# Kernel tuning notes

Measured on AMD Instinct MI355X. Metric: run time of the kernel, lower is better.

## Reference

```python
import jax, jax.numpy as jnp
import numpy as np


def _rconv(x, w, b):
    # reflection-pad 1 then 3x3 valid conv (same spatial size), NCHW/OIHW
    xp = jnp.pad(x, ((0, 0), (0, 0), (1, 1), (1, 1)), mode='reflect')
    y = jax.lax.conv_general_dilated(
        xp, w, window_strides=(1, 1), padding='VALID',
        dimension_numbers=('NCHW', 'OIHW', 'NCHW'))
    return y + b[None, :, None, None]


def setup_inputs() -> dict:
    key = jax.random.key(0)
    ks = jax.random.split(key, 12)
    B, C, H, W = 4, 256, 64, 64
    IC = 128  # inter_channels
    s = lambda fan_in: 1.0 / np.sqrt(fan_in)
    return {
        'query_feat': jax.random.normal(ks[0], (B, C, H, W), jnp.float32),
        'key_feat': jax.random.normal(ks[1], (B, C, H, W), jnp.float32),
        # 1x1 conv projections (stored as [out, in])
        'w_theta': jax.random.normal(ks[2], (IC, C), jnp.float32) * s(C),
        'b_theta': jnp.zeros((IC,), jnp.float32),
        'w_phi': jax.random.normal(ks[3], (IC, C), jnp.float32) * s(C),
        'b_phi': jnp.zeros((IC,), jnp.float32),
        # post-correlation block: conv(1->32), residual(32), conv(32->1)
        'w_in': jax.random.normal(ks[4], (32, 1, 3, 3), jnp.float32) * s(9),
        'b_in': jnp.zeros((32,), jnp.float32),
        'w_r1': jax.random.normal(ks[5], (32, 32, 3, 3), jnp.float32) * s(32 * 9),
        'b_r1': jnp.zeros((32,), jnp.float32),
        'w_r2': jax.random.normal(ks[6], (32, 32, 3, 3), jnp.float32) * s(32 * 9),
        'b_r2': jnp.zeros((32,), jnp.float32),
        'w_out': jax.random.normal(ks[7], (1, 32, 3, 3), jnp.float32) * s(32 * 9),
        'b_out': jnp.zeros((1,), jnp.float32),
    }


def reference(query_feat, key_feat, w_theta, b_theta, w_phi, b_phi,
              w_in, b_in, w_r1, b_r1, w_r2, b_r2, w_out, b_out):
    B, C, H, W = query_feat.shape
    N = H * W
    # 1x1 conv projections, flattened to sequences
    theta = jnp.einsum('oc,bchw->bohw', w_theta, query_feat) + b_theta[None, :, None, None]
    phi = jnp.einsum('oc,bchw->bohw', w_phi, key_feat) + b_phi[None, :, None, None]
    theta = theta.reshape(B, -1, N).transpose(0, 2, 1)  # [B, N, IC]
    phi = phi.reshape(B, -1, N)                          # [B, IC, N]
    # correlation matrix [B, N, N] then max over key positions
    f = jnp.matmul(theta, phi)
    sim = jnp.max(f, axis=-1).reshape(B, 1, H, W)
    # post-correlation conv refinement
    h = _rconv(sim, w_in, b_in)                      # 1 -> 32
    r = jax.nn.relu(_rconv(h, w_r1, b_r1))           # residual block
    r = _rconv(r, w_r2, b_r2)
    h = h + r
    out = _rconv(h, w_out, b_out)                    # 32 -> 1
    return out
```

## Files before the change

### kernel.cpp

```cpp
#include <hip/hip_runtime.h>

#define B_ 4
#define C_ 256
#define HH 64
#define WW 64
#define N_ 4096
#define IC_ 128
#define JC_ 16

typedef __attribute__((ext_vector_type(8))) short bf16x8;
typedef __attribute__((ext_vector_type(4))) float f32x4;

__device__ __forceinline__ short f2bf(float f) {
    unsigned u = __builtin_bit_cast(unsigned, f);
    unsigned r = (u + 0x7FFFu + ((u >> 16) & 1u)) >> 16;
    return (short)r;
}

__device__ __forceinline__ int refl(int v) {
    return v < 0 ? -v : (v > 63 ? 126 - v : v);
}

__global__ __launch_bounds__(256) void k_cvt_w(const float* __restrict__ wt,
                                               const float* __restrict__ wp,
                                               short* __restrict__ wtb,
                                               short* __restrict__ wpb) {
    int i = blockIdx.x * 256 + threadIdx.x;
    wtb[i] = f2bf(wt[i]);
    wpb[i] = f2bf(wp[i]);
}

__global__ __launch_bounds__(256) void k_project(
    const float* __restrict__ qf, const float* __restrict__ kf,
    const short* __restrict__ wq, const short* __restrict__ wk,
    const float* __restrict__ bq, const float* __restrict__ bk,
    short* __restrict__ outq, short* __restrict__ outk) {
    int z = blockIdx.z;
    const float* x = z ? kf : qf;
    const short* wbf = z ? wk : wq;
    const float* bias = z ? bk : bq;
    short* outT = z ? outk : outq;

    int b = blockIdx.y;
    int n0 = blockIdx.x * 64;
    int t = threadIdx.x;
    int lane = t & 63, wv = t >> 6;
    int l15 = lane & 15, q4 = lane >> 4;
    const float* xb = x + (size_t)b * C_ * N_;

    __shared__ float xs[2][32][65];

    f32x4 acc[8];
#pragma unroll
    for (int cf = 0; cf < 8; cf++) acc[cf] = (f32x4){0.f, 0.f, 0.f, 0.f};

    {
        int i0 = t, i1 = t + 256;
        int r0 = i0 >> 4, c0 = i0 & 15;
        int r1 = i1 >> 4, c1 = i1 & 15;
        f32x4 v0 = *(const f32x4*)(xb + (size_t)r0 * N_ + n0 + c0 * 4);
        f32x4 v1 = *(const f32x4*)(xb + (size_t)r1 * N_ + n0 + c1 * 4);
#pragma unroll
        for (int s = 0; s < 4; s++) xs[0][r0][c0 * 4 + s] = v0[s];
#pragma unroll
        for (int s = 0; s < 4; s++) xs[0][r1][c1 * 4 + s] = v1[s];
    }

    for (int ks = 0; ks < 8; ks++) {
        __syncthreads();
        int buf = ks & 1;
        if (ks < 7) {
            int cb = (ks + 1) * 32;
            int i0 = t, i1 = t + 256;
            int r0 = i0 >> 4, c0 = i0 & 15;
            int r1 = i1 >> 4, c1 = i1 & 15;
            f32x4 v0 = *(const f32x4*)(xb + (size_t)(cb + r0) * N_ + n0 + c0 * 4);
            f32x4 v1 = *(const f32x4*)(xb + (size_t)(cb + r1) * N_ + n0 + c1 * 4);
#pragma unroll
            for (int s = 0; s < 4; s++) xs[buf ^ 1][r0][c0 * 4 + s] = v0[s];
#pragma unroll
            for (int s = 0; s < 4; s++) xs[buf ^ 1][r1][c1 * 4 + s] = v1[s];
        }
        int cbase = ks * 32 + q4 * 8;
        bf16x8 a;
#pragma unroll
        for (int j = 0; j < 8; j++) a[j] = f2bf(xs[buf][q4 * 8 + j][wv * 16 + l15]);
#pragma unroll
        for (int cf = 0; cf < 8; cf++) {
            const short* wp = wbf + (cf * 16 + l15) * C_ + cbase;
            bf16x8 bfr = *(const bf16x8*)wp;
            acc[cf] = __builtin_amdgcn_mfma_f32_16x16x32_bf16(a, bfr, acc[cf], 0, 0, 0);
        }
    }
#pragma unroll
    for (int cf = 0; cf < 8; cf++) {
        int ic = cf * 16 + l15;
        float bv = bias[ic];
#pragma unroll
        for (int r = 0; r < 4; r++) {
            int n = n0 + wv * 16 + q4 * 4 + r;
            outT[((size_t)b * N_ + n) * IC_ + ic] = f2bf(acc[cf][r] + bv);
        }
    }
}

__global__ __launch_bounds__(256, 4) void k_corr(const short* __restrict__ thetaT,
                                                 const short* __restrict__ phiT,
                                                 float* __restrict__ simp) {
    __shared__ short ph[2][64][136];

    int b = blockIdx.z, jc = blockIdx.y;
    int i0 = blockIdx.x * 256;
    int t = threadIdx.x;
    int lane = t & 63, w = t >> 6;
    int l15 = lane & 15, q4 = lane >> 4;

    const short* thb = thetaT + ((size_t)b * N_ + i0 + w * 64) * IC_;
    const short* phb = phiT + ((size_t)b * N_ + jc * (N_ / JC_)) * IC_;

    bf16x8 afr[4][4];
#pragma unroll
    for (int rf = 0; rf < 4; rf++)
#pragma unroll
        for (int ks = 0; ks < 4; ks++)
            afr[rf][ks] = *(const bf16x8*)(thb + (size_t)(rf * 16 + l15) * IC_ + ks * 32 + q4 * 8);

    int srow = t >> 4, sc8 = t & 15;
#pragma unroll
    for (int k = 0; k < 4; k++)
        *(bf16x8*)(&ph[0][srow + k * 16][sc8 * 8]) =
            *(const bf16x8*)(phb + (size_t)(srow + k * 16) * IC_ + sc8 * 8);

    f32x4 rmax[4];
#pragma unroll
    for (int rf = 0; rf < 4; rf++) rmax[rf] = (f32x4){-3.0e38f, -3.0e38f, -3.0e38f, -3.0e38f};

    const int NT = (N_ / JC_) / 64;
    for (int it = 0; it < NT; it++) {
        int buf = it & 1;
        __syncthreads();
        if (it < NT - 1) {
            int j0 = (it + 1) * 64;
#pragma unroll
            for (int k = 0; k < 4; k++)
                *(bf16x8*)(&ph[buf ^ 1][srow + k * 16][sc8 * 8]) =
                    *(const bf16x8*)(phb + (size_t)(j0 + srow + k * 16) * IC_ + sc8 * 8);
        }
#pragma unroll
        for (int jf = 0; jf < 4; jf++) {
            bf16x8 bfr[4];
#pragma unroll
            for (int ks = 0; ks < 4; ks++)
                bfr[ks] = *(const bf16x8*)(&ph[buf][jf * 16 + l15][ks * 32 + q4 * 8]);
#pragma unroll
            for (int rf = 0; rf < 4; rf++) {
                f32x4 a2 = (f32x4){0.f, 0.f, 0.f, 0.f};
#pragma unroll
                for (int ks = 0; ks < 4; ks++)
                    a2 = __builtin_amdgcn_mfma_f32_16x16x32_bf16(afr[rf][ks], bfr[ks], a2, 0, 0, 0);
#pragma unroll
                for (int r = 0; r < 4; r++) rmax[rf][r] = fmaxf(rmax[rf][r], a2[r]);
            }
        }
    }

    float red[4][4];
#pragma unroll
    for (int rf = 0; rf < 4; rf++)
#pragma unroll
        for (int r = 0; r < 4; r++) {
            float v = rmax[rf][r];
            v = fmaxf(v, __shfl_xor(v, 1));
            v = fmaxf(v, __shfl_xor(v, 2));
            v = fmaxf(v, __shfl_xor(v, 4));
            v = fmaxf(v, __shfl_xor(v, 8));
            red[rf][r] = v;
        }
    if (l15 == 0) {
        float* sp = simp + ((size_t)(b * JC_ + jc)) * N_ + i0 + w * 64;
#pragma unroll
        for (int rf = 0; rf < 4; rf++)
#pragma unroll
            for (int r = 0; r < 4; r++) sp[rf * 16 + q4 * 4 + r] = red[rf][r];
    }
}

__global__ __launch_bounds__(256) void k_conv_in(const float* __restrict__ simp,
                                                 const float* __restrict__ w,
                                                 const float* __restrict__ bias,
                                                 float* __restrict__ h) {
    int y = blockIdx.x, b = blockIdx.y;
    int t = threadIdx.x;
    int oc = t >> 3, x8 = t & 7;
    __shared__ float srow[3][66];
    const float* sb = simp + (size_t)b * JC_ * N_;
    if (t < 192) {
        int r = t >> 6, x = t & 63;
        int idx = refl(y - 1 + r) * 64 + x;
        float v = -3.0e38f;
#pragma unroll
        for (int jc = 0; jc < JC_; jc++) v = fmaxf(v, sb[jc * N_ + idx]);
        srow[r][x + 1] = v;
    }
    if (t < 3) {
        int gy = refl(y - 1 + t);
        float vl = -3.0e38f, vr = -3.0e38f;
#pragma unroll
        for (int jc = 0; jc < JC_; jc++) {
            vl = fmaxf(vl, sb[jc * N_ + gy * 64 + 1]);
            vr = fmaxf(vr, sb[jc * N_ + gy * 64 + 62]);
        }
        srow[t][0] = vl;
        srow[t][65] = vr;
    }
    __syncthreads();

    float wr[9];
#pragma unroll
    for (int k = 0; k < 9; k++) wr[k] = w[oc * 9 + k];
    float bv = bias[oc];
    float acc[8];
#pragma unroll
    for (int xi = 0; xi < 8; xi++) acc[xi] = bv;
#pragma unroll
    for (int ky = 0; ky < 3; ky++)
#pragma unroll
        for (int kx = 0; kx < 3; kx++) {
            float wv2 = wr[ky * 3 + kx];
#pragma unroll
            for (int xi = 0; xi < 8; xi++) acc[xi] += wv2 * srow[ky][x8 * 8 + xi + kx];
        }
    float* op = h + (((size_t)b * 32 + oc) * 64 + y) * 64 + x8 * 8;
#pragma unroll
    for (int xi = 0; xi < 8; xi++) op[xi] = acc[xi];
}

template <bool RELU, bool ADD>
__global__ __launch_bounds__(256) void k_conv_r(const float* __restrict__ in,
                                                const float* __restrict__ w,
                                                const float* __restrict__ bias,
                                                float* __restrict__ out,
                                                const float* __restrict__ add) {
    int y = blockIdx.x, b = blockIdx.z;
    int oc0 = blockIdx.y * 16;
    int t = threadIdx.x;
    __shared__ float tile[32][3][68];

#pragma unroll
    for (int r = 0; r < 3; r++) {
        int gy = refl(y - 1 + r);
#pragma unroll
        for (int i = 0; i < 2; i++) {
            int idx = t + i * 256;
            int ic = idx >> 4, c4 = idx & 15;
            f32x4 v = *(const f32x4*)(in + (((size_t)b * 32 + ic) * 64 + gy) * 64 + c4 * 4);
#pragma unroll
            for (int s = 0; s < 4; s++) tile[ic][r][c4 * 4 + s + 1] = v[s];
        }
    }
    if (t < 96) {
        int ic = t / 3, r = t - ic * 3;
        int gy = refl(y - 1 + r);
        const float* row = in + (((size_t)b * 32 + ic) * 64 + gy) * 64;
        tile[ic][r][0] = row[1];
        tile[ic][r][65] = row[62];
    }
    __syncthreads();

    int oc = oc0 + (t >> 4), x4 = (t & 15) * 4;
    float bv = bias[oc];
    float acc[4];
#pragma unroll
    for (int xi = 0; xi < 4; xi++) acc[xi] = bv;

    for (int ic = 0; ic < 32; ic++) {
        const float* wp = w + ((size_t)oc * 32 + ic) * 9;
        float w0 = wp[0], w1 = wp[1], w2 = wp[2], w3 = wp[3], w4 = wp[4];
        float w5 = wp[5], w6 = wp[6], w7 = wp[7], w8 = wp[8];
        float xr[3][8];
#pragma unroll
        for (int r = 0; r < 3; r++) {
            const float* rowp = &tile[ic][r][x4];
            f32x4 A = *(const f32x4*)(rowp);
            f32x4 Bv = *(const f32x4*)(rowp + 4);
            xr[r][0] = A[0]; xr[r][1] = A[1]; xr[r][2] = A[2]; xr[r][3] = A[3];
            xr[r][4] = Bv[0]; xr[r][5] = Bv[1]; xr[r][6] = Bv[2]; xr[r][7] = Bv[3];
        }
#pragma unroll
        for (int xi = 0; xi < 4; xi++) {
            acc[xi] += w0 * xr[0][xi] + w1 * xr[0][xi + 1] + w2 * xr[0][xi + 2] +
                       w3 * xr[1][xi] + w4 * xr[1][xi + 1] + w5 * xr[1][xi + 2] +
                       w6 * xr[2][xi] + w7 * xr[2][xi + 1] + w8 * xr[2][xi + 2];
        }
    }
    size_t off = (((size_t)b * 32 + oc) * 64 + y) * 64 + x4;
#pragma unroll
    for (int xi = 0; xi < 4; xi++) {
        float v = acc[xi];
        if (RELU) v = fmaxf(v, 0.f);
        if (ADD) v += add[off + xi];
        out[off + xi] = v;
    }
}

__global__ __launch_bounds__(256) void k_conv_out(const float* __restrict__ hb,
                                                  const float* __restrict__ w,
                                                  const float* __restrict__ bias,
                                                  float* __restrict__ outp) {
    int y = blockIdx.x, b = blockIdx.y;
    int t = threadIdx.x;
    int x = t & 63, g = t >> 6;
    __shared__ float red[4][64];
    float acc = 0.f;
#pragma unroll
    for (int i = 0; i < 8; i++) {
        int ic = g * 8 + i;
        const float* wp = w + ic * 9;
#pragma unroll
        for (int ky = 0; ky < 3; ky++) {
            int gy = refl(y + ky - 1);
            const float* row = hb + (((size_t)b * 32 + ic) * 64 + gy) * 64;
#pragma unroll
            for (int kx = 0; kx < 3; kx++) {
                int gx = refl(x + kx - 1);
                acc += wp[ky * 3 + kx] * row[gx];
            }
        }
    }
    red[g][x] = acc;
    __syncthreads();
    if (t < 64) {
        outp[((size_t)b * 64 + y) * 64 + x] =
            bias[0] + red[0][t] + red[1][t] + red[2][t] + red[3][t];
    }
}

extern "C" void kernel_launch(void* const* d_in, const int* in_sizes, int n_in,
                              void* d_out, int out_size, void* d_ws, size_t ws_size,
                              hipStream_t stream) {
    const float* q = (const float*)d_in[0];
    const float* kf = (const float*)d_in[1];
    const float* w_theta = (const float*)d_in[2];
    const float* b_theta = (const float*)d_in[3];
    const float* w_phi = (const float*)d_in[4];
    const float* b_phi = (const float*)d_in[5];
    const float* w_in = (const float*)d_in[6];
    const float* b_in = (const float*)d_in[7];
    const float* w_r1 = (const float*)d_in[8];
    const float* b_r1 = (const float*)d_in[9];
    const float* w_r2 = (const float*)d_in[10];
    const float* b_r2 = (const float*)d_in[11];
    const float* w_out = (const float*)d_in[12];
    const float* b_out = (const float*)d_in[13];
    float* out = (float*)d_out;

    char* ws = (char*)d_ws;
    short* thetaT = (short*)(ws);
    short* phiT = (short*)(ws + 4194304);
    short* wthb = (short*)(ws + 8388608);
    short* wphb = (short*)(ws + 8454144);
    float* simp = (float*)(ws + 8519680);
    float* h = (float*)(ws);
    float* r = (float*)(ws + 2097152);

    k_cvt_w<<<128, 256, 0, stream>>>(w_theta, w_phi, wthb, wphb);
    k_project<<<dim3(64, 4, 2), 256, 0, stream>>>(q, kf, wthb, wphb, b_theta, b_phi,
                                                  thetaT, phiT);
    k_corr<<<dim3(16, JC_, 4), 256, 0, stream>>>(thetaT, phiT, simp);
    k_conv_in<<<dim3(64, 4), 256, 0, stream>>>(simp, w_in, b_in, h);
    k_conv_r<true, false><<<dim3(64, 2, 4), 256, 0, stream>>>(h, w_r1, b_r1, r, nullptr);
    k_conv_r<false, true><<<dim3(64, 2, 4), 256, 0, stream>>>(r, w_r2, b_r2, h, h);
    k_conv_out<<<dim3(64, 4), 256, 0, stream>>>(h, w_out, b_out, out);
}
```

Before: 174.9 us.

## Restructure correlation kernel to cache a 128-row phi tile and loop over theta

The correlation kernel now loads one 128-row chunk of phi into shared memory once, then loops over two 256-row theta tiles, instead of streaming 64-row phi tiles through a double buffer with a barrier per tile. The j-dimension split doubles to 32 chunks and the i-grid halves, so the launch still has 1024 blocks. This removes per-iteration synchronisation and double-buffer bookkeeping, but it gives up overlap of phi loads with MFMA work and doubles the partial-max buffer that k_conv_in must reduce.

New measurement: 226.8 us. 1.3x slower.

```diff
diff --git a/kernel.cpp b/kernel.cpp
--- a/kernel.cpp
+++ b/kernel.cpp
@@ -6,7 +6,7 @@
 #define WW 64
 #define N_ 4096
 #define IC_ 128
-#define JC_ 16
+#define JC_ 32
 
 typedef __attribute__((ext_vector_type(8))) short bf16x8;
 typedef __attribute__((ext_vector_type(4))) float f32x4;
@@ -107,51 +107,47 @@
 __global__ __launch_bounds__(256, 4) void k_corr(const short* __restrict__ thetaT,
                                                  const short* __restrict__ phiT,
                                                  float* __restrict__ simp) {
-    __shared__ short ph[2][64][136];
+    __shared__ short ph[128][136];
 
     int b = blockIdx.z, jc = blockIdx.y;
-    int i0 = blockIdx.x * 256;
     int t = threadIdx.x;
     int lane = t & 63, w = t >> 6;
     int l15 = lane & 15, q4 = lane >> 4;
 
-    const short* thb = thetaT + ((size_t)b * N_ + i0 + w * 64) * IC_;
-    const short* phb = phiT + ((size_t)b * N_ + jc * (N_ / JC_)) * IC_;
-
-    bf16x8 afr[4][4];
-#pragma unroll
-    for (int rf = 0; rf < 4; rf++)
-#pragma unroll
-        for (int ks = 0; ks < 4; ks++)
-            afr[rf][ks] = *(const bf16x8*)(thb + (size_t)(rf * 16 + l15) * IC_ + ks * 32 + q4 * 8);
-
-    int srow = t >> 4, sc8 = t & 15;
-#pragma unroll
-    for (int k = 0; k < 4; k++)
-        *(bf16x8*)(&ph[0][srow + k * 16][sc8 * 8]) =
-            *(const bf16x8*)(phb + (size_t)(srow + k * 16) * IC_ + sc8 * 8);
-
-    f32x4 rmax[4];
-#pragma unroll
-    for (int rf = 0; rf < 4; rf++) rmax[rf] = (f32x4){-3.0e38f, -3.0e38f, -3.0e38f, -3.0e38f};
-
-    const int NT = (N_ / JC_) / 64;
-    for (int it = 0; it < NT; it++) {
-        int buf = it & 1;
-        __syncthreads();
-        if (it < NT - 1) {
-            int j0 = (it + 1) * 64;
-#pragma unroll
-            for (int k = 0; k < 4; k++)
-                *(bf16x8*)(&ph[buf ^ 1][srow + k * 16][sc8 * 8]) =
-                    *(const bf16x8*)(phb + (size_t)(j0 + srow + k * 16) * IC_ + sc8 * 8);
-        }
-#pragma unroll
-        for (int jf = 0; jf < 4; jf++) {
+    const short* phb = phiT + ((size_t)b * N_ + jc * 128) * IC_;
+
+#pragma unroll
+    for (int k = 0; k < 8; k++) {
+        int id = t + k * 256;
+        int row = id >> 4, c8 = id & 15;
+        *(bf16x8*)(&ph[row][c8 * 8]) =
+            *(const bf16x8*)(phb + (size_t)row * IC_ + c8 * 8);
+    }
+    __syncthreads();
+
+    for (int ti = 0; ti < 2; ti++) {
+        int i0 = blockIdx.x * 512 + ti * 256;
+        const short* thb = thetaT + ((size_t)b * N_ + i0 + w * 64) * IC_;
+
+        bf16x8 afr[4][4];
+#pragma unroll
+        for (int rf = 0; rf < 4; rf++)
+#pragma unroll
+            for (int ks = 0; ks < 4; ks++)
+                afr[rf][ks] =
+                    *(const bf16x8*)(thb + (size_t)(rf * 16 + l15) * IC_ + ks * 32 + q4 * 8);
+
+        f32x4 rmax[4];
+#pragma unroll
+        for (int rf = 0; rf < 4; rf++)
+            rmax[rf] = (f32x4){-3.0e38f, -3.0e38f, -3.0e38f, -3.0e38f};
+
+#pragma unroll
+        for (int jf = 0; jf < 8; jf++) {
             bf16x8 bfr[4];
 #pragma unroll
             for (int ks = 0; ks < 4; ks++)
-                bfr[ks] = *(const bf16x8*)(&ph[buf][jf * 16 + l15][ks * 32 + q4 * 8]);
+                bfr[ks] = *(const bf16x8*)(&ph[jf * 16 + l15][ks * 32 + q4 * 8]);
 #pragma unroll
             for (int rf = 0; rf < 4; rf++) {
                 f32x4 a2 = (f32x4){0.f, 0.f, 0.f, 0.f};
@@ -162,26 +158,26 @@
                 for (int r = 0; r < 4; r++) rmax[rf][r] = fmaxf(rmax[rf][r], a2[r]);
             }
         }
-    }
-
-    float red[4][4];
-#pragma unroll
-    for (int rf = 0; rf < 4; rf++)
-#pragma unroll
-        for (int r = 0; r < 4; r++) {
-            float v = rmax[rf][r];
-            v = fmaxf(v, __shfl_xor(v, 1));
-            v = fmaxf(v, __shfl_xor(v, 2));
-            v = fmaxf(v, __shfl_xor(v, 4));
-            v = fmaxf(v, __shfl_xor(v, 8));
-            red[rf][r] = v;
-        }
-    if (l15 == 0) {
-        float* sp = simp + ((size_t)(b * JC_ + jc)) * N_ + i0 + w * 64;
-#pragma unroll
-        for (int rf = 0; rf < 4; rf++)
-#pragma unroll
-            for (int r = 0; r < 4; r++) sp[rf * 16 + q4 * 4 + r] = red[rf][r];
+
+#pragma unroll
+        for (int rf = 0; rf < 4; rf++) {
+#pragma unroll
+            for (int r = 0; r < 4; r++) {
+                float v = rmax[rf][r];
+                v = fmaxf(v, __shfl_xor(v, 1));
+                v = fmaxf(v, __shfl_xor(v, 2));
+                v = fmaxf(v, __shfl_xor(v, 4));
+                v = fmaxf(v, __shfl_xor(v, 8));
+                rmax[rf][r] = v;
+            }
+        }
+        if (l15 == 0) {
+            float* sp = simp + ((size_t)(b * JC_ + jc)) * N_ + i0 + w * 64;
+#pragma unroll
+            for (int rf = 0; rf < 4; rf++)
+#pragma unroll
+                for (int r = 0; r < 4; r++) sp[rf * 16 + q4 * 4 + r] = rmax[rf][r];
+        }
     }
 }
 
@@ -366,7 +362,7 @@
     k_cvt_w<<<128, 256, 0, stream>>>(w_theta, w_phi, wthb, wphb);
     k_project<<<dim3(64, 4, 2), 256, 0, stream>>>(q, kf, wthb, wphb, b_theta, b_phi,
                                                   thetaT, phiT);
-    k_corr<<<dim3(16, JC_, 4), 256, 0, stream>>>(thetaT, phiT, simp);
+    k_corr<<<dim3(8, JC_, 4), 256, 0, stream>>>(thetaT, phiT, simp);
     k_conv_in<<<dim3(64, 4), 256, 0, stream>>>(simp, w_in, b_in, h);
     k_conv_r<true, false><<<dim3(64, 2, 4), 256, 0, stream>>>(h, w_r1, b_r1, r, nullptr);
     k_conv_r<false, true><<<dim3(64, 2, 4), 256, 0, stream>>>(r, w_r2, b_r2, h, h);
```
